# Kernel tuning notes

Measured on AMD Instinct MI355X. Metric: run time of the kernel, lower is better.

The kernel has to match this reference:

```python
import jax, jax.numpy as jnp
import numpy as np

K = 1024       # num mixture components
D = 6          # state_dim (pos + vel)
B = 16384      # number of query points


def setup_inputs() -> dict:
    key = jax.random.key(0)
    k1, k2, k3, k4 = jax.random.split(key, 4)
    x = jax.random.normal(k1, (B, D), dtype=jnp.float32)
    means = jax.random.normal(k2, (K, D), dtype=jnp.float32)
    # SPD covariances: F @ F^T / D + 0.1 * I
    F = jax.random.normal(k3, (K, D, D), dtype=jnp.float32)
    covs = jnp.einsum('kij,klj->kil', F, F) / D + 0.1 * jnp.eye(D, dtype=jnp.float32)
    w = jax.random.uniform(k4, (K,), dtype=jnp.float32, minval=0.1, maxval=1.0)
    weights = w / jnp.sum(w)
    return {"x": x, "means": means, "covs": covs, "weights": weights}


def reference(x, means, covs, weights):
    """Batched GMM.log_pdf: for each point x_b, logsumexp_k [log w_k + log N(x_b; mu_k, Sigma_k)].
    Same math as the equinox module (Cholesky + triangular solve per component),
    vectorized over both components and query points.
    Returns log_pdf of shape [B]."""
    L = jnp.linalg.cholesky(covs)                      # [K, D, D]
    diff = x[:, None, :] - means[None, :, :]           # [B, K, D]
    # Solve L_k y = diff for all points at once: b has shape [K, D, B]
    b = jnp.transpose(diff, (1, 2, 0))                 # [K, D, B]
    y = jax.scipy.linalg.solve_triangular(L, b, lower=True)  # [K, D, B]
    quad = jnp.sum(y * y, axis=1)                      # [K, B]
    log_det = 2.0 * jnp.sum(jnp.log(jnp.diagonal(L, axis1=-2, axis2=-1)), axis=-1)  # [K]
    k_dim = means.shape[-1]
    log_prob = -0.5 * (k_dim * jnp.log(2.0 * jnp.pi) + log_det[:, None] + quad)      # [K, B]
    log_comp = jnp.log(weights)[:, None] + log_prob    # [K, B]
    return jax.scipy.special.logsumexp(log_comp, axis=0)  # [B]
```

## Files before the change

### kernel.cpp

```cpp
#include <hip/hip_runtime.h>
#include <hip/hip_bf16.h>
#include <math.h>

#define KCOMP 1024
#define DDIM  6
#define BPTS  16384

#define PTS    64
#define NWAVE  16
#define NTPW   4

typedef __attribute__((ext_vector_type(8))) short bf16x8;
typedef __attribute__((ext_vector_type(4))) float f32x4;

__device__ __forceinline__ unsigned short f32_to_bf16(float f) {
    unsigned int u = __float_as_uint(f);
    u += 0x7fffu + ((u >> 16) & 1u);
    return (unsigned short)(u >> 16);
}
__device__ __forceinline__ float bf16_to_f32(unsigned short h) {
    return __uint_as_float(((unsigned int)h) << 16);
}

__global__ __launch_bounds__(64, 1) void gmm_precompute(
        const float* __restrict__ means,
        const float* __restrict__ covs,
        const float* __restrict__ weights,
        unsigned short* __restrict__ Wh,
        unsigned short* __restrict__ Wl) {
    int k = blockIdx.x * 64 + threadIdx.x;
    if (k >= KCOMP) return;

    float A[6][6];
    const float* C = covs + k * 36;
    #pragma unroll
    for (int i = 0; i < 6; i++)
        #pragma unroll
        for (int j = 0; j < 6; j++)
            A[i][j] = C[i * 6 + j];

    float logdet = 0.0f;
    #pragma unroll
    for (int j = 0; j < 6; j++) {
        float d = A[j][j];
        #pragma unroll
        for (int t = 0; t < 6; t++) if (t < j) d -= A[j][t] * A[j][t];
        float ljj = sqrtf(d);
        logdet += logf(ljj);
        A[j][j] = ljj;
        float inv = 1.0f / ljj;
        #pragma unroll
        for (int i = 0; i < 6; i++) {
            if (i > j) {
                float s = A[i][j];
                #pragma unroll
                for (int t = 0; t < 6; t++) if (t < j) s -= A[i][t] * A[j][t];
                A[i][j] = s * inv;
            }
        }
    }
    logdet *= 2.0f;

    float Li[6][6];
    #pragma unroll
    for (int j = 0; j < 6; j++) {
        Li[j][j] = 1.0f / A[j][j];
        #pragma unroll
        for (int i = 0; i < 6; i++) {
            if (i > j) {
                float s = 0.0f;
                #pragma unroll
                for (int t = 0; t < 6; t++) if (t >= j && t < i) s += A[i][t] * Li[t][j];
                Li[i][j] = -s * (1.0f / A[i][i]);
            }
        }
    }

    #pragma unroll
    for (int i = 0; i < 6; i++) {
        #pragma unroll
        for (int j = 0; j < 6; j++) {
            if (j >= i) {
                float s = 0.0f;
                int lo = (i > j) ? i : j;
                #pragma unroll
                for (int t = 0; t < 6; t++) if (t >= lo) s += Li[t][i] * Li[t][j];
                A[i][j] = s;
                A[j][i] = s;
            }
        }
    }

    const float* mu = means + k * 6;
    float m[6];
    #pragma unroll
    for (int i = 0; i < 6; i++) m[i] = mu[i];

    float b[6];
    float muPmu = 0.0f;
    #pragma unroll
    for (int i = 0; i < 6; i++) {
        float s = 0.0f;
        #pragma unroll
        for (int j = 0; j < 6; j++) s += A[i][j] * m[j];
        b[i] = s;
        muPmu += s * m[i];
    }

    const float LOG_2PI = 1.8378770664093453f;
    const float LOG2E   = 1.4426950408889634f;
    float c = logf(weights[k]) - 0.5f * (6.0f * LOG_2PI + logdet) - 0.5f * muPmu;

    float wv[32];
    int t = 0;
    #pragma unroll
    for (int i = 0; i < 6; i++)
        #pragma unroll
        for (int j = 0; j < 6; j++)
            if (j >= i) wv[t++] = LOG2E * ((i == j) ? -0.5f * A[i][j] : -A[i][j]);
    #pragma unroll
    for (int i = 0; i < 6; i++) wv[t++] = LOG2E * b[i];
    wv[27] = LOG2E * c;
    wv[28] = 0.0f; wv[29] = 0.0f; wv[30] = 0.0f; wv[31] = 0.0f;

    int ntile = k >> 4, n15 = k & 15;
    #pragma unroll
    for (int kk = 0; kk < 32; kk++) {
        float v = wv[kk];
        unsigned short h = f32_to_bf16(v);
        unsigned short l = f32_to_bf16(v - bf16_to_f32(h));
        int idx = ((ntile * 64) + ((kk >> 3) << 4) + n15) * 8 + (kk & 7);
        Wh[idx] = h;
        Wl[idx] = l;
    }
}

__global__ __launch_bounds__(1024, 4) void gmm_main(
        const float* __restrict__ x,
        const unsigned short* __restrict__ Wh,
        const unsigned short* __restrict__ Wl,
        float* __restrict__ out) {
    const int tid  = threadIdx.x;
    const int lane = tid & 63;
    const int w    = __builtin_amdgcn_readfirstlane(tid >> 6);
    const int quad = lane >> 4;
    const int m15  = lane & 15;
    const int pbase = blockIdx.x * PTS;

    float xv[4][6];
    #pragma unroll
    for (int pt = 0; pt < 4; pt++) {
        const float* xp = x + (pbase + pt * 16 + m15) * 6;
        #pragma unroll
        for (int i = 0; i < 6; i++) xv[pt][i] = xp[i];
    }

    float f[4][8];
    if (quad == 0) {
        #pragma unroll
        for (int pt = 0; pt < 4; pt++) {
            const float* v = xv[pt];
            f[pt][0]=v[0]*v[0]; f[pt][1]=v[0]*v[1]; f[pt][2]=v[0]*v[2]; f[pt][3]=v[0]*v[3];
            f[pt][4]=v[0]*v[4]; f[pt][5]=v[0]*v[5]; f[pt][6]=v[1]*v[1]; f[pt][7]=v[1]*v[2];
        }
    } else if (quad == 1) {
        #pragma unroll
        for (int pt = 0; pt < 4; pt++) {
            const float* v = xv[pt];
            f[pt][0]=v[1]*v[3]; f[pt][1]=v[1]*v[4]; f[pt][2]=v[1]*v[5]; f[pt][3]=v[2]*v[2];
            f[pt][4]=v[2]*v[3]; f[pt][5]=v[2]*v[4]; f[pt][6]=v[2]*v[5]; f[pt][7]=v[3]*v[3];
        }
    } else if (quad == 2) {
        #pragma unroll
        for (int pt = 0; pt < 4; pt++) {
            const float* v = xv[pt];
            f[pt][0]=v[3]*v[4]; f[pt][1]=v[3]*v[5]; f[pt][2]=v[4]*v[4]; f[pt][3]=v[4]*v[5];
            f[pt][4]=v[5]*v[5]; f[pt][5]=v[0];      f[pt][6]=v[1];      f[pt][7]=v[2];
        }
    } else {
        #pragma unroll
        for (int pt = 0; pt < 4; pt++) {
            const float* v = xv[pt];
            f[pt][0]=v[3]; f[pt][1]=v[4]; f[pt][2]=v[5]; f[pt][3]=1.0f;
            f[pt][4]=0.0f; f[pt][5]=0.0f; f[pt][6]=0.0f; f[pt][7]=0.0f;
        }
    }

    bf16x8 Ah[4], Al[4];
    #pragma unroll
    for (int pt = 0; pt < 4; pt++) {
        #pragma unroll
        for (int j = 0; j < 8; j++) {
            float v = f[pt][j];
            unsigned short h = f32_to_bf16(v);
            unsigned short l = f32_to_bf16(v - bf16_to_f32(h));
            Ah[pt][j] = (short)h;
            Al[pt][j] = (short)l;
        }
    }

    const bf16x8* WhF = (const bf16x8*)Wh + (w * NTPW) * 64;
    const bf16x8* WlF = (const bf16x8*)Wl + (w * NTPW) * 64;

    float esum[4][4];
    #pragma unroll
    for (int pt = 0; pt < 4; pt++)
        #pragma unroll
        for (int r = 0; r < 4; r++) esum[pt][r] = 0.0f;

    #pragma unroll
    for (int t = 0; t < NTPW; t++) {
        bf16x8 bh = WhF[t * 64 + lane];
        bf16x8 bl = WlF[t * 64 + lane];
        #pragma unroll
        for (int pt = 0; pt < 4; pt++) {
            f32x4 c = {0.0f, 0.0f, 0.0f, 0.0f};
            c = __builtin_amdgcn_mfma_f32_16x16x32_bf16(Ah[pt], bh, c, 0, 0, 0);
            c = __builtin_amdgcn_mfma_f32_16x16x32_bf16(Al[pt], bh, c, 0, 0, 0);
            c = __builtin_amdgcn_mfma_f32_16x16x32_bf16(Ah[pt], bl, c, 0, 0, 0);
            #pragma unroll
            for (int r = 0; r < 4; r++)
                esum[pt][r] += __builtin_amdgcn_exp2f(c[r]);
        }
    }

    #pragma unroll
    for (int pt = 0; pt < 4; pt++) {
        #pragma unroll
        for (int r = 0; r < 4; r++) {
            float v = esum[pt][r];
            v += __shfl_xor(v, 1);
            v += __shfl_xor(v, 2);
            v += __shfl_xor(v, 4);
            v += __shfl_xor(v, 8);
            esum[pt][r] = v;
        }
    }

    __shared__ float partial[NWAVE][PTS];
    if (m15 == 0) {
        #pragma unroll
        for (int pt = 0; pt < 4; pt++)
            #pragma unroll
            for (int r = 0; r < 4; r++)
                partial[w][pt * 16 + quad * 4 + r] = esum[pt][r];
    }
    __syncthreads();

    if (tid < PTS) {
        float S = 0.0f;
        #pragma unroll
        for (int c = 0; c < NWAVE; c++) S += partial[c][tid];
        const float LN2 = 0.6931471805599453f;
        out[pbase + tid] = LN2 * __builtin_amdgcn_logf(S);
    }
}

extern "C" void kernel_launch(void* const* d_in, const int* in_sizes, int n_in,
                              void* d_out, int out_size, void* d_ws, size_t ws_size,
                              hipStream_t stream) {
    const float* x       = (const float*)d_in[0];
    const float* means   = (const float*)d_in[1];
    const float* covs    = (const float*)d_in[2];
    const float* weights = (const float*)d_in[3];
    float* out = (float*)d_out;

    unsigned short* Wh = (unsigned short*)d_ws;
    unsigned short* Wl = Wh + 32768;

    gmm_precompute<<<KCOMP / 64, 64, 0, stream>>>(means, covs, weights, Wh, Wl);
    gmm_main<<<BPTS / PTS, 1024, 0, stream>>>(x, Wh, Wl, out);
}
```

Baseline: 68.70 us.

## Build A fragments once per block in shared memory; use fast intrinsics in precompute

In the main kernel, all 16 waves previously each loaded x and computed the same quadratic-feature bf16 hi/lo fragments for the block's 64 points. Now 8 waves each build one fragment (point tile × hi/lo split), write it to LDS, and after a barrier every wave reads all of them. This removes 16x redundant global loads and conversion ALU work, at the cost of an extra __syncthreads and 8 KB of LDS. The precompute kernel also switches to hardware sqrt/rcp/log2 intrinsics and takes one log of the product of the diagonal, with the constant folded into base 2.

```diff
diff --git a/kernel.cpp b/kernel.cpp
--- a/kernel.cpp
+++ b/kernel.cpp
@@ -39,16 +39,16 @@
         for (int j = 0; j < 6; j++)
             A[i][j] = C[i * 6 + j];
 
-    float logdet = 0.0f;
+    float dprod = 1.0f;
     #pragma unroll
     for (int j = 0; j < 6; j++) {
         float d = A[j][j];
         #pragma unroll
         for (int t = 0; t < 6; t++) if (t < j) d -= A[j][t] * A[j][t];
-        float ljj = sqrtf(d);
-        logdet += logf(ljj);
+        float ljj = __builtin_amdgcn_sqrtf(d);
+        dprod *= ljj;
         A[j][j] = ljj;
-        float inv = 1.0f / ljj;
+        float inv = __builtin_amdgcn_rcpf(ljj);
         #pragma unroll
         for (int i = 0; i < 6; i++) {
             if (i > j) {
@@ -59,19 +59,19 @@
             }
         }
     }
-    logdet *= 2.0f;
+    float logdet2 = 2.0f * __builtin_amdgcn_logf(dprod);
 
     float Li[6][6];
     #pragma unroll
     for (int j = 0; j < 6; j++) {
-        Li[j][j] = 1.0f / A[j][j];
+        Li[j][j] = __builtin_amdgcn_rcpf(A[j][j]);
         #pragma unroll
         for (int i = 0; i < 6; i++) {
             if (i > j) {
                 float s = 0.0f;
                 #pragma unroll
                 for (int t = 0; t < 6; t++) if (t >= j && t < i) s += A[i][t] * Li[t][j];
-                Li[i][j] = -s * (1.0f / A[i][i]);
+                Li[i][j] = -s * __builtin_amdgcn_rcpf(A[i][i]);
             }
         }
     }
@@ -107,9 +107,11 @@
         muPmu += s * m[i];
     }
 
-    const float LOG_2PI = 1.8378770664093453f;
-    const float LOG2E   = 1.4426950408889634f;
-    float c = logf(weights[k]) - 0.5f * (6.0f * LOG_2PI + logdet) - 0.5f * muPmu;
+    const float LOG2_2PI = 2.6514961294723187f;
+    const float LOG2E    = 1.4426950408889634f;
+    float c2 = __builtin_amdgcn_logf(weights[k])
+             - 0.5f * (6.0f * LOG2_2PI + logdet2)
+             - 0.5f * LOG2E * muPmu;
 
     float wv[32];
     int t = 0;
@@ -120,7 +122,7 @@
             if (j >= i) wv[t++] = LOG2E * ((i == j) ? -0.5f * A[i][j] : -A[i][j]);
     #pragma unroll
     for (int i = 0; i < 6; i++) wv[t++] = LOG2E * b[i];
-    wv[27] = LOG2E * c;
+    wv[27] = c2;
     wv[28] = 0.0f; wv[29] = 0.0f; wv[30] = 0.0f; wv[31] = 0.0f;
 
     int ntile = k >> 4, n15 = k & 15;
@@ -147,56 +149,48 @@
     const int m15  = lane & 15;
     const int pbase = blockIdx.x * PTS;
 
-    float xv[4][6];
+    __shared__ bf16x8 fragA[8][64];
+    __shared__ float  partial[NWAVE][PTS];
+
+    if (w < 8) {
+        const int pt    = w & 3;
+        const int split = w >> 2;
+        float v[6];
+        const float* xp = x + (pbase + pt * 16 + m15) * 6;
+        #pragma unroll
+        for (int i = 0; i < 6; i++) v[i] = xp[i];
+
+        float f[8];
+        if (quad == 0) {
+            f[0]=v[0]*v[0]; f[1]=v[0]*v[1]; f[2]=v[0]*v[2]; f[3]=v[0]*v[3];
+            f[4]=v[0]*v[4]; f[5]=v[0]*v[5]; f[6]=v[1]*v[1]; f[7]=v[1]*v[2];
+        } else if (quad == 1) {
+            f[0]=v[1]*v[3]; f[1]=v[1]*v[4]; f[2]=v[1]*v[5]; f[3]=v[2]*v[2];
+            f[4]=v[2]*v[3]; f[5]=v[2]*v[4]; f[6]=v[2]*v[5]; f[7]=v[3]*v[3];
+        } else if (quad == 2) {
+            f[0]=v[3]*v[4]; f[1]=v[3]*v[5]; f[2]=v[4]*v[4]; f[3]=v[4]*v[5];
+            f[4]=v[5]*v[5]; f[5]=v[0];      f[6]=v[1];      f[7]=v[2];
+        } else {
+            f[0]=v[3]; f[1]=v[4]; f[2]=v[5]; f[3]=1.0f;
+            f[4]=0.0f; f[5]=0.0f; f[6]=0.0f; f[7]=0.0f;
+        }
+
+        bf16x8 frag;
+        #pragma unroll
+        for (int j = 0; j < 8; j++) {
+            unsigned short h = f32_to_bf16(f[j]);
+            frag[j] = (split == 0) ? (short)h
+                                   : (short)f32_to_bf16(f[j] - bf16_to_f32(h));
+        }
+        fragA[w][lane] = frag;
+    }
+    __syncthreads();
+
+    bf16x8 Ah[4], Al[4];
     #pragma unroll
     for (int pt = 0; pt < 4; pt++) {
-        const float* xp = x + (pbase + pt * 16 + m15) * 6;
-        #pragma unroll
-        for (int i = 0; i < 6; i++) xv[pt][i] = xp[i];
-    }
-
-    float f[4][8];
-    if (quad == 0) {
-        #pragma unroll
-        for (int pt = 0; pt < 4; pt++) {
-            const float* v = xv[pt];
-            f[pt][0]=v[0]*v[0]; f[pt][1]=v[0]*v[1]; f[pt][2]=v[0]*v[2]; f[pt][3]=v[0]*v[3];
-            f[pt][4]=v[0]*v[4]; f[pt][5]=v[0]*v[5]; f[pt][6]=v[1]*v[1]; f[pt][7]=v[1]*v[2];
-        }
-    } else if (quad == 1) {
-        #pragma unroll
-        for (int pt = 0; pt < 4; pt++) {
-            const float* v = xv[pt];
-            f[pt][0]=v[1]*v[3]; f[pt][1]=v[1]*v[4]; f[pt][2]=v[1]*v[5]; f[pt][3]=v[2]*v[2];
-            f[pt][4]=v[2]*v[3]; f[pt][5]=v[2]*v[4]; f[pt][6]=v[2]*v[5]; f[pt][7]=v[3]*v[3];
-        }
-    } else if (quad == 2) {
-        #pragma unroll
-        for (int pt = 0; pt < 4; pt++) {
-            const float* v = xv[pt];
-            f[pt][0]=v[3]*v[4]; f[pt][1]=v[3]*v[5]; f[pt][2]=v[4]*v[4]; f[pt][3]=v[4]*v[5];
-            f[pt][4]=v[5]*v[5]; f[pt][5]=v[0];      f[pt][6]=v[1];      f[pt][7]=v[2];
-        }
-    } else {
-        #pragma unroll
-        for (int pt = 0; pt < 4; pt++) {
-            const float* v = xv[pt];
-            f[pt][0]=v[3]; f[pt][1]=v[4]; f[pt][2]=v[5]; f[pt][3]=1.0f;
-            f[pt][4]=0.0f; f[pt][5]=0.0f; f[pt][6]=0.0f; f[pt][7]=0.0f;
-        }
-    }
-
-    bf16x8 Ah[4], Al[4];
-    #pragma unroll
-    for (int pt = 0; pt < 4; pt++) {
-        #pragma unroll
-        for (int j = 0; j < 8; j++) {
-            float v = f[pt][j];
-            unsigned short h = f32_to_bf16(v);
-            unsigned short l = f32_to_bf16(v - bf16_to_f32(h));
-            Ah[pt][j] = (short)h;
-            Al[pt][j] = (short)l;
-        }
+        Ah[pt] = fragA[pt][lane];
+        Al[pt] = fragA[4 + pt][lane];
     }
 
     const bf16x8* WhF = (const bf16x8*)Wh + (w * NTPW) * 64;
@@ -237,7 +231,6 @@
         }
     }
 
-    __shared__ float partial[NWAVE][PTS];
     if (m15 == 0) {
         #pragma unroll
         for (int pt = 0; pt < 4; pt++)
```

Result: faster. 66.96 us (-2.5%).
